# Optimization experiments

Hardware: AMD Instinct MI355X
Metric: run time of the kernel (lower is better)

Reference implementation:

```python
import jax, jax.numpy as jnp
import numpy as np
import math

NUM_HEADS = 8
LN_EPS = 1e-5
SINK_EPS = 1.0  # entropic eps in SinkhornDistance (eps=1)


def _layer_norm(x, g, b):
    m = jnp.mean(x, axis=-1, keepdims=True)
    v = jnp.var(x, axis=-1, keepdims=True)
    return (x - m) * jax.lax.rsqrt(v + LN_EPS) * g + b


def setup_inputs() -> dict:
    key = jax.random.key(0)
    ks = jax.random.split(key, 8)
    B, n, dQ, dV = 8, 1024, 512, 512
    s = 1.0 / math.sqrt(dV)
    return {
        "Q": jax.random.normal(ks[0], (B, n, dQ), jnp.float32),
        "K": jax.random.normal(ks[1], (B, n, dQ), jnp.float32),
        "Wq": jax.random.normal(ks[2], (dV, dQ), jnp.float32) * s,
        "bq": jax.random.normal(ks[3], (dV,), jnp.float32) * 0.01,
        "Wo": jax.random.normal(ks[4], (dV, dV), jnp.float32) * s,
        "bo": jax.random.normal(ks[5], (dV,), jnp.float32) * 0.01,
        "g0": jnp.ones((dV,), jnp.float32),
        "b0": jnp.zeros((dV,), jnp.float32),
        "g1": jnp.ones((dV,), jnp.float32),
        "b1": jnp.zeros((dV,), jnp.float32),
    }


def reference(Q, K, Wq, bq, Wo, bo, g0, b0, g1, b1):
    # K is accepted by the original forward but unused (K_ = V_ = Q_).
    B, n, _ = Q.shape
    dim_V = Wq.shape[0]
    H = NUM_HEADS
    d = dim_V // H

    Qp = Q @ Wq.T + bq                                   # [B, n, dim_V]
    # torch.cat(Q.split(d, 2), 0): head-major stacking -> [H*B, n, d]
    Q_ = Qp.reshape(B, n, H, d).transpose(2, 0, 1, 3).reshape(H * B, n, d)

    sqrtV = math.sqrt(math.sqrt(dim_V))
    X = Q_ / sqrtV
    # cost = dotmat(X, X) = -X X^T  (overall scaled by 1/sqrt(dim_V))
    C = -jnp.einsum('bnd,bmd->bnm', X, X)                # [HB, n, n]

    # log-domain Sinkhorn, eps=1, max_iter=1, mu = nu = 1/n
    log_mu = jnp.log(1.0 / n + 1e-8).astype(Q.dtype)
    M0 = -C / SINK_EPS
    u = SINK_EPS * (log_mu - jax.scipy.special.logsumexp(M0, axis=-1))         # [HB, n]
    v = SINK_EPS * (log_mu - jax.scipy.special.logsumexp(
        (-C + u[:, :, None]) / SINK_EPS, axis=1))                               # [HB, n]
    pi = jnp.exp((-C + u[:, :, None] + v[:, None, :]) / SINK_EPS)               # [HB, n, n]

    A = pi * n
    O_ = Q_ + jnp.einsum('bnm,bmd->bnd', A, Q_)          # [HB, n, d]
    # inverse head stacking -> [B, n, dim_V]
    O = O_.reshape(H, B, n, d).transpose(1, 2, 0, 3).reshape(B, n, dim_V)

    O = _layer_norm(O, g0, b0)
    O = O + jax.nn.relu(O @ Wo.T + bo)
    O = _layer_norm(O, g1, b1)
    return O
```

## Files before the change

kernel.cpp:

```cpp
#include <hip/hip_runtime.h>
#include <hip/hip_bf16.h>

typedef __bf16 bf16;
typedef __bf16 bf16x4 __attribute__((ext_vector_type(4)));
typedef __bf16 bf16x8 __attribute__((ext_vector_type(8)));
typedef float  f32x4  __attribute__((ext_vector_type(4)));
typedef float  f32x16 __attribute__((ext_vector_type(16)));
typedef unsigned int uint32x2 __attribute__((ext_vector_type(2)));

#define DEVI static __device__ __forceinline__

constexpr float SCALE_S = 0.04419417382415922f;
constexpr float SCALE2  = 0.063758716f;
constexpr float L2MU    = -9.9999852f;
constexpr int   LDT     = 72;

DEVI f32x4 mfma16(bf16x8 a, bf16x8 b, f32x4 c) {
    return __builtin_amdgcn_mfma_f32_16x16x32_bf16(a, b, c, 0, 0, 0);
}
DEVI f32x16 mfma32(bf16x8 a, bf16x8 b, f32x16 c) {
    return __builtin_amdgcn_mfma_f32_32x32x16_bf16(a, b, c, 0, 0, 0);
}
DEVI unsigned cvtpk(float lo, float hi) {
    unsigned r;
    asm("v_cvt_pk_bf16_f32 %0, %1, %2" : "=v"(r) : "v"(lo), "v"(hi));
    return r;
}

DEVI bf16x8 cvt8(const float* __restrict__ p) {
    const float4 f0 = *(const float4*)p;
    const float4 f1 = *(const float4*)(p + 4);
    bf16x8 h;
    h[0] = (bf16)f0.x; h[1] = (bf16)f0.y; h[2] = (bf16)f0.z; h[3] = (bf16)f0.w;
    h[4] = (bf16)f1.x; h[5] = (bf16)f1.y; h[6] = (bf16)f1.z; h[7] = (bf16)f1.w;
    return h;
}

template<int EPI>
__global__ __launch_bounds__(256)
void gemm_kernel(const void* __restrict__ Ap, const float* __restrict__ Bm,
                 const float* __restrict__ bias, const bf16* __restrict__ X0,
                 bf16* __restrict__ outQh, bf16* __restrict__ outQhT,
                 float* __restrict__ outT)
{
    __shared__ bf16 sA[64 * LDT];
    __shared__ bf16 sB[64 * LDT];
    const int tid = threadIdx.x;
    const int rowBase = blockIdx.y * 64;
    const int colBase = blockIdx.x * 64;
    const int w = tid >> 6, lane = tid & 63, quad = lane >> 4, l16 = lane & 15;
    const int wr = (w >> 1) * 32, wc = (w & 1) * 32;

    f32x4 acc[2][2];
    #pragma unroll
    for (int i = 0; i < 2; ++i)
        #pragma unroll
        for (int j = 0; j < 2; ++j)
            #pragma unroll
            for (int e = 0; e < 4; ++e) acc[i][j][e] = 0.f;

    for (int kt = 0; kt < 512; kt += 64) {
        if (kt) __syncthreads();
        #pragma unroll
        for (int it = 0; it < 2; ++it) {
            int idx = it * 256 + tid;
            int r = idx >> 3, kb = idx & 7;
            if (EPI == 0) {
                *(bf16x8*)(&sA[r * LDT + kb * 8]) =
                    cvt8((const float*)Ap + (size_t)(rowBase + r) * 512 + kt + kb * 8);
            } else {
                *(uint4*)(&sA[r * LDT + kb * 8]) =
                    *(const uint4*)((const bf16*)Ap + (size_t)(rowBase + r) * 512 + kt + kb * 8);
            }
            *(bf16x8*)(&sB[r * LDT + kb * 8]) =
                cvt8(Bm + (size_t)(colBase + r) * 512 + kt + kb * 8);
        }
        __syncthreads();
        #pragma unroll
        for (int kk = 0; kk < 2; ++kk) {
            bf16x8 a[2], b[2];
            #pragma unroll
            for (int i = 0; i < 2; ++i)
                a[i] = *(const bf16x8*)(&sA[(wr + i * 16 + l16) * LDT + kk * 32 + quad * 8]);
            #pragma unroll
            for (int j = 0; j < 2; ++j)
                b[j] = *(const bf16x8*)(&sB[(wc + j * 16 + l16) * LDT + kk * 32 + quad * 8]);
            #pragma unroll
            for (int i = 0; i < 2; ++i)
                #pragma unroll
                for (int j = 0; j < 2; ++j)
                    acc[i][j] = mfma16(a[i], b[j], acc[i][j]);
        }
    }

    #pragma unroll
    for (int i = 0; i < 2; ++i) {
        #pragma unroll
        for (int j = 0; j < 2; ++j) {
            const int col = colBase + wc + j * 16 + l16;
            const float bv = bias[col];
            if (EPI == 0) {
                const int hh = col >> 6, jj = col & 63;
                const int rowA = rowBase + wr + i * 16 + quad * 4;
                const int bb = rowA >> 10, iib = rowA & 1023;
                const int bhh = (hh << 3) + bb;
                bf16x4 pk;
                #pragma unroll
                for (int rg = 0; rg < 4; ++rg) {
                    const float z = acc[i][j][rg] + bv;
                    pk[rg] = (bf16)z;
                    outQh[((size_t)(bhh * 1024 + iib + rg) << 6) + jj] = (bf16)z;
                }
                if (outQhT)
                    *(bf16x4*)(&outQhT[(((size_t)bhh * 64 + jj) << 10) + iib]) = pk;
            } else {
                #pragma unroll
                for (int rg = 0; rg < 4; ++rg) {
                    const int row = rowBase + wr + i * 16 + quad * 4 + rg;
                    const float z = acc[i][j][rg] + bv;
                    const float x0 = (float)X0[(size_t)row * 512 + col];
                    outT[(size_t)row * 512 + col] = x0 + fmaxf(z, 0.f);
                }
            }
        }
    }
}

template<int ADD_U>
__global__ __launch_bounds__(256, 4)
void sink_lse_kernel(const bf16* __restrict__ Qh, const float* __restrict__ uin,
                     float* __restrict__ out)
{
    __shared__ bf16 sQi[128 * LDT];
    __shared__ bf16 sQm[2][64 * LDT];
    __shared__ float su[1024];
    const int tid = threadIdx.x;
    const int lin = blockIdx.y * 8 + blockIdx.x;
    const int wk  = ((lin & 7) << 6) | (lin >> 3);
    const int bh = wk >> 3;
    const int rowTile = (wk & 7) * 128;
    const bf16* Qb = Qh + ((size_t)bh << 16);

    #pragma unroll
    for (int it = 0; it < 4; ++it) {
        int idx = it * 256 + tid;
        int r = idx >> 3, kb = idx & 7;
        *(uint4*)(&sQi[r * LDT + kb * 8]) =
            *(const uint4*)(Qb + ((rowTile + r) << 6) + kb * 8);
    }
    if (ADD_U)
        *(float4*)(&su[tid * 4]) = *(const float4*)(uin + (bh << 10) + tid * 4);

    const int r0 = tid >> 3, kb0 = tid & 7;
    #pragma unroll
    for (int it = 0; it < 2; ++it)
        *(uint4*)(&sQm[0][(it * 32 + r0) * LDT + kb0 * 8]) =
            *(const uint4*)(Qb + ((it * 32 + r0) << 6) + kb0 * 8);
    __syncthreads();

    const int w = tid >> 6, lane = tid & 63, quad = lane >> 4, l16 = lane & 15;
    float rsum[2][4] = {{0.f,0.f,0.f,0.f},{0.f,0.f,0.f,0.f}};

    for (int mt = 0; mt < 16; ++mt) {
        const int cur = mt & 1;
        uint4 pf[2];
        if (mt < 15) {
            #pragma unroll
            for (int it = 0; it < 2; ++it)
                pf[it] = *(const uint4*)(Qb + (((mt + 1) * 64 + it * 32 + r0) << 6) + kb0 * 8);
        }

        f32x4 acc[2][4];
        #pragma unroll
        for (int a = 0; a < 2; ++a)
            #pragma unroll
            for (int ct = 0; ct < 4; ++ct)
                #pragma unroll
                for (int e = 0; e < 4; ++e) acc[a][ct][e] = 0.f;

        #pragma unroll
        for (int kk = 0; kk < 2; ++kk) {
            bf16x8 afr[2], bfr[4];
            #pragma unroll
            for (int a = 0; a < 2; ++a)
                afr[a] = *(const bf16x8*)(&sQi[(w * 32 + a * 16 + l16) * LDT + kk * 32 + quad * 8]);
            #pragma unroll
            for (int ct = 0; ct < 4; ++ct)
                bfr[ct] = *(const bf16x8*)(&sQm[cur][(ct * 16 + l16) * LDT + kk * 32 + quad * 8]);
            #pragma unroll
            for (int a = 0; a < 2; ++a)
                #pragma unroll
                for (int ct = 0; ct < 4; ++ct)
                    acc[a][ct] = mfma16(afr[a], bfr[ct], acc[a][ct]);
        }
        #pragma unroll
        for (int a = 0; a < 2; ++a)
            #pragma unroll
            for (int ct = 0; ct < 4; ++ct) {
                const float uadd = ADD_U ? su[mt * 64 + ct * 16 + l16] : 0.f;
                #pragma unroll
                for (int rg = 0; rg < 4; ++rg)
                    rsum[a][rg] += __builtin_amdgcn_exp2f(
                        fmaf(acc[a][ct][rg], SCALE2, uadd));
            }

        if (mt < 15) {
            #pragma unroll
            for (int it = 0; it < 2; ++it)
                *(uint4*)(&sQm[cur ^ 1][(it * 32 + r0) * LDT + kb0 * 8]) = pf[it];
        }
        __syncthreads();
    }
    #pragma unroll
    for (int off = 1; off < 16; off <<= 1)
        #pragma unroll
        for (int a = 0; a < 2; ++a)
            #pragma unroll
            for (int rg = 0; rg < 4; ++rg)
                rsum[a][rg] += __shfl_xor(rsum[a][rg], off);

    if (l16 == 0) {
        #pragma unroll
        for (int a = 0; a < 2; ++a)
            #pragma unroll
            for (int rg = 0; rg < 4; ++rg)
                out[(bh << 10) + rowTile + w * 32 + a * 16 + quad * 4 + rg] =
                    L2MU - __builtin_amdgcn_logf(rsum[a][rg]);
    }
}

template<int USE_T>
__global__ __launch_bounds__(256, 2)
void sink_av_kernel(const bf16* __restrict__ Qh, const bf16* __restrict__ QhT,
                    const float* __restrict__ u, const float* __restrict__ v,
                    float* __restrict__ O)
{
    __shared__ bf16 sQi[128 * LDT];
    __shared__ bf16 sQm[2][64 * LDT];
    __shared__ bf16 sQmT[2][64 * LDT];
    __shared__ float sv[1024];
    const int tid = threadIdx.x;
    const int lin = blockIdx.y * 8 + blockIdx.x;
    const int wk  = ((lin & 7) << 6) | (lin >> 3);
    const int bh = wk >> 3;
    const int rowTile = (wk & 7) * 128;
    const bf16* Qb = Qh + ((size_t)bh << 16);
    const bf16* QbT = QhT + ((size_t)bh << 16);
    const int w = tid >> 6, lane = tid & 63, hi = lane >> 5, l31 = lane & 31;
    const int r0 = tid >> 3, kb0 = tid & 7;

    #pragma unroll
    for (int it = 0; it < 4; ++it) {
        int idx = it * 256 + tid;
        int r = idx >> 3, kb = idx & 7;
        *(uint4*)(&sQi[r * LDT + kb * 8]) =
            *(const uint4*)(Qb + ((rowTile + r) << 6) + kb * 8);
    }
    *(float4*)(&sv[tid * 4]) = *(const float4*)(v + (bh << 10) + tid * 4);
    const float u2p = u[(bh << 10) + rowTile + w * 32 + l31] + 10.f;

    #pragma unroll
    for (int it = 0; it < 2; ++it) {
        const int r = it * 32 + r0;
        uint4 val = *(const uint4*)(Qb + (r << 6) + kb0 * 8);
        *(uint4*)(&sQm[0][r * LDT + kb0 * 8]) = val;
        if (USE_T) {
            *(uint4*)(&sQmT[0][r * LDT + kb0 * 8]) =
                *(const uint4*)(QbT + (r << 10) + kb0 * 8);
        } else {
            union { uint4 q; bf16 e[8]; } cv; cv.q = val;
            #pragma unroll
            for (int j = 0; j < 8; ++j)
                sQmT[0][(kb0 * 8 + j) * LDT + r] = cv.e[j];
        }
    }
    __syncthreads();

    f32x16 accO[2];
    #pragma unroll
    for (int dt = 0; dt < 2; ++dt)
        #pragma unroll
        for (int e = 0; e < 16; ++e) accO[dt][e] = 0.f;

    for (int mt = 0; mt < 16; ++mt) {
        const int cur = mt & 1;
        uint4 pfm[2], pft[2];
        if (mt < 15) {
            #pragma unroll
            for (int it = 0; it < 2; ++it) {
                const int r = it * 32 + r0;
                pfm[it] = *(const uint4*)(Qb + (((mt + 1) * 64 + r) << 6) + kb0 * 8);
                if (USE_T)
                    pft[it] = *(const uint4*)(QbT + (r << 10) + (mt + 1) * 64 + kb0 * 8);
            }
        }

        f32x16 accT[2];
        #pragma unroll
        for (int t = 0; t < 2; ++t)
            #pragma unroll
            for (int e = 0; e < 16; ++e) accT[t][e] = 0.f;
        #pragma unroll
        for (int ks = 0; ks < 4; ++ks) {
            const bf16x8 bq = *(const bf16x8*)(&sQi[(w * 32 + l31) * LDT + ks * 16 + hi * 8]);
            #pragma unroll
            for (int t = 0; t < 2; ++t) {
                const bf16x8 am = *(const bf16x8*)(&sQm[cur][(t * 32 + l31) * LDT + ks * 16 + hi * 8]);
                accT[t] = mfma32(am, bq, accT[t]);
            }
        }

        bf16x8 pa[4];
        #pragma unroll
        for (int t = 0; t < 2; ++t) {
            f32x4 vf[4];
            #pragma unroll
            for (int g = 0; g < 4; ++g)
                vf[g] = *(const f32x4*)(&sv[mt * 64 + t * 32 + g * 8 + hi * 4]);
            float p[16];
            #pragma unroll
            for (int r = 0; r < 16; ++r)
                p[r] = __builtin_amdgcn_exp2f(
                         fmaf(accT[t][r], SCALE2, u2p + vf[r >> 2][r & 3]));
            #pragma unroll
            for (int kk = 0; kk < 2; ++kk) {
                const int rb = kk * 8;
                unsigned X0 = cvtpk(p[rb + 0], p[rb + 1]);
                unsigned Y0 = cvtpk(p[rb + 4], p[rb + 5]);
                unsigned X1 = cvtpk(p[rb + 2], p[rb + 3]);
                unsigned Y1 = cvtpk(p[rb + 6], p[rb + 7]);
                uint32x2 s0 = __builtin_amdgcn_permlane32_swap(X0, Y0, false, false);
                uint32x2 s1 = __builtin_amdgcn_permlane32_swap(X1, Y1, false, false);
                union { unsigned wd[4]; bf16x8 v8; } u4;
                u4.wd[0] = s0[0]; u4.wd[1] = s1[0]; u4.wd[2] = s0[1]; u4.wd[3] = s1[1];
                pa[t * 2 + kk] = u4.v8;
            }
        }

        #pragma unroll
        for (int ks = 0; ks < 4; ++ks)
            #pragma unroll
            for (int dt = 0; dt < 2; ++dt) {
                const bf16x8 bt = *(const bf16x8*)(&sQmT[cur][(dt * 32 + l31) * LDT + ks * 16 + hi * 8]);
                accO[dt] = mfma32(pa[ks], bt, accO[dt]);
            }

        if (mt < 15) {
            #pragma unroll
            for (int it = 0; it < 2; ++it) {
                const int r = it * 32 + r0;
                *(uint4*)(&sQm[cur ^ 1][r * LDT + kb0 * 8]) = pfm[it];
                if (USE_T) {
                    *(uint4*)(&sQmT[cur ^ 1][r * LDT + kb0 * 8]) = pft[it];
                } else {
                    union { uint4 q; bf16 e[8]; } cv; cv.q = pfm[it];
                    #pragma unroll
                    for (int j = 0; j < 8; ++j)
                        sQmT[cur ^ 1][(kb0 * 8 + j) * LDT + r] = cv.e[j];
                }
            }
        }
        __syncthreads();
    }

    const int hh = bh >> 3, bb = bh & 7;
    #pragma unroll
    for (int dt = 0; dt < 2; ++dt) {
        const int dcol = dt * 32 + l31;
        #pragma unroll
        for (int r = 0; r < 16; ++r) {
            const int irow = w * 32 + (r & 3) + 8 * (r >> 2) + 4 * hi;
            const float o = (float)sQi[irow * LDT + dcol] + accO[dt][r];
            O[((size_t)(bb * 1024 + rowTile + irow) << 9) + (hh << 6) + dcol] = o;
        }
    }
}

template<typename OutT>
__global__ __launch_bounds__(256)
void ln_kernel(const float* __restrict__ X, const float* __restrict__ g,
               const float* __restrict__ bb, OutT* __restrict__ out)
{
    const int row = blockIdx.x;
    const float* x = X + (size_t)row * 512;
    const float2 v2 = ((const float2*)x)[threadIdx.x];
    float s  = v2.x + v2.y;
    float ss = v2.x * v2.x + v2.y * v2.y;
    #pragma unroll
    for (int off = 32; off; off >>= 1) {
        s  += __shfl_down(s, off);
        ss += __shfl_down(ss, off);
    }
    __shared__ float red[8];
    const int w = threadIdx.x >> 6, lane = threadIdx.x & 63;
    if (lane == 0) { red[w] = s; red[4 + w] = ss; }
    __syncthreads();
    s  = red[0] + red[1] + red[2] + red[3];
    ss = red[4] + red[5] + red[6] + red[7];
    const float mean = s * (1.f / 512.f);
    const float var  = ss * (1.f / 512.f) - mean * mean;
    const float rstd = rsqrtf(var + 1e-5f);
    const int c = threadIdx.x * 2;
    const float y0 = (v2.x - mean) * rstd * g[c]     + bb[c];
    const float y1 = (v2.y - mean) * rstd * g[c + 1] + bb[c + 1];
    out[(size_t)row * 512 + c]     = (OutT)y0;
    out[(size_t)row * 512 + c + 1] = (OutT)y1;
}

extern "C" void kernel_launch(void* const* d_in, const int* in_sizes, int n_in,
                              void* d_out, int out_size, void* d_ws, size_t ws_size,
                              hipStream_t stream)
{
    const float* Q  = (const float*)d_in[0];
    const float* Wq = (const float*)d_in[2];
    const float* bq = (const float*)d_in[3];
    const float* Wo = (const float*)d_in[4];
    const float* bo = (const float*)d_in[5];
    const float* g0 = (const float*)d_in[6];
    const float* b0 = (const float*)d_in[7];
    const float* g1 = (const float*)d_in[8];
    const float* b1 = (const float*)d_in[9];

    char* ws = (char*)d_ws;
    const bool useT = ws_size >= (size_t)34078720;

    bf16 *Qh, *QhT, *X0;
    float *u, *v, *Obuf;
    if (useT) {
        Qh   = (bf16*)ws;
        QhT  = (bf16*)(ws + 8388608);
        X0   = (bf16*)(ws + 8388608);
        u    = (float*)(ws + 16777216);
        v    = (float*)(ws + 17039360);
        Obuf = (float*)(ws + 17301504);
    } else {
        Qh   = (bf16*)ws;
        QhT  = nullptr;
        X0   = (bf16*)ws;
        u    = (float*)(ws + 8388608);
        v    = (float*)(ws + 8650752);
        Obuf = (float*)(ws + 8912896);
    }

    gemm_kernel<0><<<dim3(8, 128), 256, 0, stream>>>(Q, Wq, bq, nullptr, Qh, QhT, nullptr);
    sink_lse_kernel<0><<<dim3(8, 64), 256, 0, stream>>>(Qh, nullptr, u);
    sink_lse_kernel<1><<<dim3(8, 64), 256, 0, stream>>>(Qh, u, v);
    if (useT)
        sink_av_kernel<1><<<dim3(8, 64), 256, 0, stream>>>(Qh, QhT, u, v, Obuf);
    else
        sink_av_kernel<0><<<dim3(8, 64), 256, 0, stream>>>(Qh, Qh, u, v, Obuf);
    ln_kernel<bf16><<<8192, 256, 0, stream>>>(Obuf, g0, b0, X0);
    gemm_kernel<1><<<dim3(8, 128), 256, 0, stream>>>(X0, Wo, bo, X0, nullptr, nullptr, Obuf);
    ln_kernel<float><<<8192, 256, 0, stream>>>(Obuf, g1, b1, (float*)d_out);
}
```

Baseline: 207.8 us.

## Halve LSE row tile, keep query fragments in registers, swizzle GEMM block order

The Sinkhorn log-sum-exp kernel now processes 64 query rows per block instead of 128, doubling the grid, and loads each wave's A fragments straight from global memory into registers instead of staging them in shared memory. This cuts LDS use and per-thread accumulators, aiming for higher occupancy and more blocks to spread across CUs, at the cost of re-streaming the key tiles twice as often. The GEMM kernel also remaps block indices so that consecutive blocks share row tiles, which is meant to improve L2 locality.

```diff
diff --git a/kernel.cpp b/kernel.cpp
--- a/kernel.cpp
+++ b/kernel.cpp
@@ -10,7 +10,6 @@
 
 #define DEVI static __device__ __forceinline__
 
-constexpr float SCALE_S = 0.04419417382415922f;
 constexpr float SCALE2  = 0.063758716f;
 constexpr float L2MU    = -9.9999852f;
 constexpr int   LDT     = 72;
@@ -46,8 +45,10 @@
     __shared__ bf16 sA[64 * LDT];
     __shared__ bf16 sB[64 * LDT];
     const int tid = threadIdx.x;
-    const int rowBase = blockIdx.y * 64;
-    const int colBase = blockIdx.x * 64;
+    const int lin = blockIdx.y * 8 + blockIdx.x;
+    const int wk  = ((lin & 7) << 7) | (lin >> 3);
+    const int rowBase = (wk >> 3) * 64;
+    const int colBase = (wk & 7) * 64;
     const int w = tid >> 6, lane = tid & 63, quad = lane >> 4, l16 = lane & 15;
     const int wr = (w >> 1) * 32, wc = (w & 1) * 32;
 
@@ -131,23 +132,15 @@
 void sink_lse_kernel(const bf16* __restrict__ Qh, const float* __restrict__ uin,
                      float* __restrict__ out)
 {
-    __shared__ bf16 sQi[128 * LDT];
     __shared__ bf16 sQm[2][64 * LDT];
     __shared__ float su[1024];
     const int tid = threadIdx.x;
-    const int lin = blockIdx.y * 8 + blockIdx.x;
-    const int wk  = ((lin & 7) << 6) | (lin >> 3);
-    const int bh = wk >> 3;
-    const int rowTile = (wk & 7) * 128;
+    const int lin = blockIdx.y * 16 + blockIdx.x;
+    const int wk  = ((lin & 7) << 7) | (lin >> 3);
+    const int bh = wk >> 4;
+    const int rowTile = (wk & 15) * 64;
     const bf16* Qb = Qh + ((size_t)bh << 16);
 
-    #pragma unroll
-    for (int it = 0; it < 4; ++it) {
-        int idx = it * 256 + tid;
-        int r = idx >> 3, kb = idx & 7;
-        *(uint4*)(&sQi[r * LDT + kb * 8]) =
-            *(const uint4*)(Qb + ((rowTile + r) << 6) + kb * 8);
-    }
     if (ADD_U)
         *(float4*)(&su[tid * 4]) = *(const float4*)(uin + (bh << 10) + tid * 4);
 
@@ -156,10 +149,15 @@
     for (int it = 0; it < 2; ++it)
         *(uint4*)(&sQm[0][(it * 32 + r0) * LDT + kb0 * 8]) =
             *(const uint4*)(Qb + ((it * 32 + r0) << 6) + kb0 * 8);
+
+    const int w = tid >> 6, lane = tid & 63, quad = lane >> 4, l16 = lane & 15;
+    bf16x8 afr[2];
+    #pragma unroll
+    for (int kk = 0; kk < 2; ++kk)
+        afr[kk] = *(const bf16x8*)(Qb + ((rowTile + w * 16 + l16) << 6) + kk * 32 + quad * 8);
     __syncthreads();
 
-    const int w = tid >> 6, lane = tid & 63, quad = lane >> 4, l16 = lane & 15;
-    float rsum[2][4] = {{0.f,0.f,0.f,0.f},{0.f,0.f,0.f,0.f}};
+    float rsum[4] = {0.f, 0.f, 0.f, 0.f};
 
     for (int mt = 0; mt < 16; ++mt) {
         const int cur = mt & 1;
@@ -170,39 +168,29 @@
                 pf[it] = *(const uint4*)(Qb + (((mt + 1) * 64 + it * 32 + r0) << 6) + kb0 * 8);
         }
 
-        f32x4 acc[2][4];
-        #pragma unroll
-        for (int a = 0; a < 2; ++a)
-            #pragma unroll
-            for (int ct = 0; ct < 4; ++ct)
-                #pragma unroll
-                for (int e = 0; e < 4; ++e) acc[a][ct][e] = 0.f;
+        f32x4 acc[4];
+        #pragma unroll
+        for (int ct = 0; ct < 4; ++ct)
+            #pragma unroll
+            for (int e = 0; e < 4; ++e) acc[ct][e] = 0.f;
 
         #pragma unroll
         for (int kk = 0; kk < 2; ++kk) {
-            bf16x8 afr[2], bfr[4];
-            #pragma unroll
-            for (int a = 0; a < 2; ++a)
-                afr[a] = *(const bf16x8*)(&sQi[(w * 32 + a * 16 + l16) * LDT + kk * 32 + quad * 8]);
+            bf16x8 bfr[4];
             #pragma unroll
             for (int ct = 0; ct < 4; ++ct)
                 bfr[ct] = *(const bf16x8*)(&sQm[cur][(ct * 16 + l16) * LDT + kk * 32 + quad * 8]);
             #pragma unroll
-            for (int a = 0; a < 2; ++a)
-                #pragma unroll
-                for (int ct = 0; ct < 4; ++ct)
-                    acc[a][ct] = mfma16(afr[a], bfr[ct], acc[a][ct]);
-        }
-        #pragma unroll
-        for (int a = 0; a < 2; ++a)
-            #pragma unroll
-            for (int ct = 0; ct < 4; ++ct) {
-                const float uadd = ADD_U ? su[mt * 64 + ct * 16 + l16] : 0.f;
-                #pragma unroll
-                for (int rg = 0; rg < 4; ++rg)
-                    rsum[a][rg] += __builtin_amdgcn_exp2f(
-                        fmaf(acc[a][ct][rg], SCALE2, uadd));
-            }
+            for (int ct = 0; ct < 4; ++ct)
+                acc[ct] = mfma16(afr[kk], bfr[ct], acc[ct]);
+        }
+        #pragma unroll
+        for (int ct = 0; ct < 4; ++ct) {
+            const float uadd = ADD_U ? su[mt * 64 + ct * 16 + l16] : 0.f;
+            #pragma unroll
+            for (int rg = 0; rg < 4; ++rg)
+                rsum[rg] += __builtin_amdgcn_exp2f(fmaf(acc[ct][rg], SCALE2, uadd));
+        }
 
         if (mt < 15) {
             #pragma unroll
@@ -214,18 +202,14 @@
     #pragma unroll
     for (int off = 1; off < 16; off <<= 1)
         #pragma unroll
-        for (int a = 0; a < 2; ++a)
-            #pragma unroll
-            for (int rg = 0; rg < 4; ++rg)
-                rsum[a][rg] += __shfl_xor(rsum[a][rg], off);
+        for (int rg = 0; rg < 4; ++rg)
+            rsum[rg] += __shfl_xor(rsum[rg], off);
 
     if (l16 == 0) {
         #pragma unroll
-        for (int a = 0; a < 2; ++a)
-            #pragma unroll
-            for (int rg = 0; rg < 4; ++rg)
-                out[(bh << 10) + rowTile + w * 32 + a * 16 + quad * 4 + rg] =
-                    L2MU - __builtin_amdgcn_logf(rsum[a][rg]);
+        for (int rg = 0; rg < 4; ++rg)
+            out[(bh << 10) + rowTile + w * 16 + quad * 4 + rg] =
+                L2MU - __builtin_amdgcn_logf(rsum[rg]);
     }
 }
 
@@ -443,8 +427,8 @@
     }
 
     gemm_kernel<0><<<dim3(8, 128), 256, 0, stream>>>(Q, Wq, bq, nullptr, Qh, QhT, nullptr);
-    sink_lse_kernel<0><<<dim3(8, 64), 256, 0, stream>>>(Qh, nullptr, u);
-    sink_lse_kernel<1><<<dim3(8, 64), 256, 0, stream>>>(Qh, u, v);
+    sink_lse_kernel<0><<<dim3(16, 64), 256, 0, stream>>>(Qh, nullptr, u);
+    sink_lse_kernel<1><<<dim3(16, 64), 256, 0, stream>>>(Qh, u, v);
     if (useT)
         sink_av_kernel<1><<<dim3(8, 64), 256, 0, stream>>>(Qh, QhT, u, v, Obuf);
     else
```

Result: faster. 203.8 us (-2.0%).
